# Optimization experiments

Measured on AMD Instinct MI355X. Metric: run time of the kernel, lower is better.

## Reference

```python
import jax, jax.numpy as jnp
import numpy as np

B, S, D = 1, 4096, 512
INNER = 512
K, PAD = 3, 1
MAX_OUT = 4 * S  # static padded output length (torch uses data-dependent max)
EPS = 1e-5
TINY_SLOWDOWN = 0.5


def _conv1d(x, w, b):
    # x: [B, C_in, S], w: [C_out, C_in, K] -> [B, C_out, S]
    y = jax.lax.conv_general_dilated(x, w, window_strides=(1,), padding=[(PAD, PAD)],
                                     dimension_numbers=('NCH', 'OIH', 'NCH'))
    return y + b[None, :, None]


def _layernorm(x, g, b):
    m = jnp.mean(x, axis=-1, keepdims=True)
    v = jnp.var(x, axis=-1, keepdims=True)
    return (x - m) * jax.lax.rsqrt(v + EPS) * g + b


def _duration_predictor(enc, c1w, c1b, g1, b1, c2w, c2b, g2, b2, lw, lb):
    # enc: [B, S, D]; dropout is identity (eval mode)
    x = _conv1d(enc.transpose(0, 2, 1), c1w, c1b).transpose(0, 2, 1)   # [B,S,INNER]
    x = jax.nn.relu(_layernorm(x, g1, b1))
    x = _conv1d(x.transpose(0, 2, 1), c2w, c2b).transpose(0, 2, 1)     # [B,S,INNER]
    x = jax.nn.relu(_layernorm(x, g2, b2))
    out = jax.nn.relu(jnp.einsum('bsd,od->bso', x, lw) + lb)           # [B,S,1]
    return out[..., 0]                                                  # [B,S] (B==1 => matches squeeze/unsqueeze(0))


def setup_inputs() -> dict:
    key = jax.random.key(0)
    ks = jax.random.split(key, 4)
    return {
        'enc_output': jax.random.normal(ks[0], (B, S, D), dtype=jnp.float32),
        'conv1_w': jax.random.normal(ks[1], (INNER, D, K), dtype=jnp.float32) * 0.02,
        'conv1_b': jnp.zeros((INNER,), jnp.float32),
        'ln1_g': jnp.ones((INNER,), jnp.float32),
        'ln1_b': jnp.zeros((INNER,), jnp.float32),
        'conv2_w': jax.random.normal(ks[2], (INNER, INNER, K), dtype=jnp.float32) * 0.02,
        'conv2_b': jnp.zeros((INNER,), jnp.float32),
        'ln2_g': jnp.ones((INNER,), jnp.float32),
        'ln2_b': jnp.zeros((INNER,), jnp.float32),
        'lin_w': jax.random.normal(ks[3], (1, INNER), jnp.float32) * 0.1,
        'lin_b': jnp.zeros((1,), jnp.float32),
    }


def reference(enc_output, conv1_w, conv1_b, ln1_g, ln1_b, conv2_w, conv2_b,
              ln2_g, ln2_b, lin_w, lin_b):
    pred = _duration_predictor(enc_output, conv1_w, conv1_b, ln1_g, ln1_b,
                               conv2_w, conv2_b, ln2_g, ln2_b, lin_w, lin_b)
    dur = jnp.floor(pred + TINY_SLOWDOWN).astype(jnp.int32)            # [B,S], nonneg so floor == int()
    cum = jnp.cumsum(dur, axis=-1)                                     # [B,S]
    t = jnp.arange(MAX_OUT, dtype=jnp.int32)                           # [T]
    # frame t belongs to phoneme i where cum[i-1] <= t < cum[i]
    idx = jax.vmap(lambda c: jnp.searchsorted(c, t, side='right'))(cum)  # [B,T]
    valid = t[None, :] < cum[:, -1:]                                   # [B,T]
    idx = jnp.clip(idx, 0, S - 1)
    gathered = jnp.take_along_axis(enc_output, idx[:, :, None], axis=1)  # [B,T,D]
    mod_enc_output = jnp.where(valid[:, :, None], gathered, jnp.zeros((), enc_output.dtype))
    output_pos = jnp.arange(1, MAX_OUT + 1, dtype=jnp.int64 if jax.config.jax_enable_x64 else jnp.int32)[None, :]
    return mod_enc_output, output_pos
```

## Files before the change

kernel.cpp:

```cpp
#include <hip/hip_runtime.h>

#define S      4096
#define D      512
#define KWIN   3
#define SP     (S + 2)
#define MAXOUT 16384
#define EPSLN  1e-5f
#define NIT    16
#define NKT    48
#define NPAIR  24

typedef __attribute__((ext_vector_type(8))) short short8;
typedef __attribute__((ext_vector_type(4))) float floatx4;

__device__ inline ushort f2bf(float x) {
  union { float f; unsigned u; } v; v.f = x;
  unsigned r = v.u + 0x7fffu + ((v.u >> 16) & 1u);
  return (ushort)(r >> 16);
}
__device__ inline float bf2f(ushort h) {
  union { float f; unsigned u; } v; v.u = ((unsigned)h) << 16;
  return v.f;
}

#define PBX 1025
#define PBW 384

__global__ __launch_bounds__(256) void pack_all_kernel(
    const float* __restrict__ x, const float* __restrict__ w1,
    const float* __restrict__ w2, ushort* __restrict__ Xph,
    ushort* __restrict__ Xpl, ushort* __restrict__ B1h, ushort* __restrict__ B1l,
    ushort* __restrict__ B2h, ushort* __restrict__ B2l,
    ushort* __restrict__ T1h, ushort* __restrict__ T1l) {
  const int b = blockIdx.x;
  if (b < PBX) {
    const int v = b * 256 + threadIdx.x;
    if (v >= SP * 64) return;
    const int g   = v >> 6;
    const int oct = v & 63;
    const int i0  = oct * 8;
    float vv[8];
    if (g == 0 || g == SP - 1) {
#pragma unroll
      for (int j = 0; j < 8; ++j) vv[j] = 0.f;
    } else {
      const float4 a = *(const float4*)(x + (size_t)(g - 1) * D + i0);
      const float4 c = *(const float4*)(x + (size_t)(g - 1) * D + i0 + 4);
      vv[0] = a.x; vv[1] = a.y; vv[2] = a.z; vv[3] = a.w;
      vv[4] = c.x; vv[5] = c.y; vv[6] = c.z; vv[7] = c.w;
    }
    short8 h8, l8;
#pragma unroll
    for (int j = 0; j < 8; ++j) {
      const ushort hi = f2bf(vv[j]);
      h8[j] = (short)hi;
      l8[j] = (short)f2bf(vv[j] - bf2f(hi));
    }
    const size_t dst = ((size_t)(oct >> 2) * SP + g) * 32 + (size_t)(oct & 3) * 8;
    *(short8*)(Xph + dst) = h8;
    *(short8*)(Xpl + dst) = l8;
  } else if (b < PBX + 2 * PBW) {
    const int wsel = (b - PBX) >= PBW;
    const int u = ((b - PBX) - (wsel ? PBW : 0)) * 256 + threadIdx.x;
    const float* __restrict__ w = wsel ? w2 : w1;
    ushort* __restrict__ bh = wsel ? B2h : B1h;
    ushort* __restrict__ bl = wsel ? B2l : B1l;
    const int kk0 = (u & 3) * 8;
    const int o   = (u >> 2) & 511;
    const int it  = (u >> 11) & 15;
    const int k   = u >> 15;
    const float* __restrict__ src =
        w + (size_t)o * (D * KWIN) + (size_t)(it * 32 + kk0) * KWIN + k;
    short8 h8, l8;
#pragma unroll
    for (int j = 0; j < 8; ++j) {
      const float vv = src[j * KWIN];
      const ushort hi = f2bf(vv);
      h8[j] = (short)hi;
      l8[j] = (short)f2bf(vv - bf2f(hi));
    }
    const size_t idx = (size_t)kk0 + ((size_t)o << 5) + ((size_t)it << 14) +
                       ((size_t)k << 18);
    *(short8*)(bh + idx) = h8;
    *(short8*)(bl + idx) = l8;
  } else {
    const int z = threadIdx.x;
    if (z < 128) {
      const int c    = z >> 3;
      const int rr   = (z >> 2) & 1;
      const int colo = (z & 3) * 8;
      const size_t off = ((size_t)c * SP + (rr ? (SP - 1) : 0)) * 32 + colo;
      short8 zero = {};
      *(short8*)(T1h + off) = zero;
      *(short8*)(T1l + off) = zero;
    }
  }
}

#define TM 128
#define TN 64
#define AH_OFF 0
#define AL_OFF 8192
#define BH_OFF 16384
#define BL_OFF 20480
#define DBUFSZ 24576

__device__ inline void gload16(const void* g, void* l) {
  __builtin_amdgcn_global_load_lds((const __attribute__((address_space(1))) void*)g,
                                   (__attribute__((address_space(3))) void*)l,
                                   16, 0, 0);
}

__global__ __launch_bounds__(512) void gemm_mfma_kernel(
    const ushort* __restrict__ Ah, const ushort* __restrict__ Al,
    const ushort* __restrict__ Bh, const ushort* __restrict__ Bl,
    float* __restrict__ C) {
  __shared__ __align__(16) ushort smem[2 * DBUFSZ];

  const int tid  = threadIdx.x;
  const int wave = tid >> 6;
  const int lane = tid & 63;
  const int row0 = blockIdx.x * TM;
  const int col0 = blockIdx.y * TN;
  const int wm0  = (wave >> 1) * 32;
  const int wn0  = (wave & 1) * 32;
  const int fr   = lane & 15;
  const int quad = lane >> 4;

  floatx4 acc[2][2] = {};

  auto stage = [&](int p, int db) {
    ushort* base = smem + db * DBUFSZ;
    if (wave < 4) {
      const int sub = wave & 1;
      const int kt  = 2 * p + sub;
      const int tap   = kt >> 4;
      const int itile = kt & 15;
      const ushort* gb = (wave < 2 ? Ah : Al) +
                         ((size_t)itile * SP + row0 + tap) * 32;
      ushort* lb = base + (wave < 2 ? AH_OFF : AL_OFF) + sub * 4096;
#pragma unroll
      for (int seg = 0; seg < 8; ++seg)
        gload16(gb + seg * 512 + lane * 8, lb + seg * 512);
    } else if (wave < 6) {
      const ushort* src = (wave == 4 ? Bh : Bl);
      ushort* lb0 = base + (wave == 4 ? BH_OFF : BL_OFF);
#pragma unroll
      for (int sub = 0; sub < 2; ++sub) {
        const int kt = 2 * p + sub;
        const ushort* gb = src + ((size_t)kt * D + col0) * 32;
#pragma unroll
        for (int seg = 0; seg < 4; ++seg)
          gload16(gb + seg * 512 + lane * 8, lb0 + sub * 2048 + seg * 512);
      }
    }
  };

  stage(0, 0);

  for (int p = 0; p < NPAIR; ++p) {
    const int db = p & 1;
    __syncthreads();
    if (p + 1 < NPAIR) stage(p + 1, db ^ 1);

#pragma unroll
    for (int sub = 0; sub < 2; ++sub) {
      short8 ah[2], al2[2], bh[2], bl2[2];
#pragma unroll
      for (int mf = 0; mf < 2; ++mf) {
        const int off = sub * 4096 + (wm0 + mf * 16 + fr) * 32 + quad * 8;
        ah[mf]  = *(const short8*)&smem[db * DBUFSZ + AH_OFF + off];
        al2[mf] = *(const short8*)&smem[db * DBUFSZ + AL_OFF + off];
      }
#pragma unroll
      for (int nf = 0; nf < 2; ++nf) {
        const int offb = sub * 2048 + (wn0 + nf * 16 + fr) * 32 + quad * 8;
        bh[nf]  = *(const short8*)&smem[db * DBUFSZ + BH_OFF + offb];
        bl2[nf] = *(const short8*)&smem[db * DBUFSZ + BL_OFF + offb];
      }
#pragma unroll
      for (int mf = 0; mf < 2; ++mf)
#pragma unroll
        for (int nf = 0; nf < 2; ++nf) {
          acc[mf][nf] = __builtin_amdgcn_mfma_f32_16x16x32_bf16(ah[mf],  bh[nf],  acc[mf][nf], 0, 0, 0);
          acc[mf][nf] = __builtin_amdgcn_mfma_f32_16x16x32_bf16(ah[mf],  bl2[nf], acc[mf][nf], 0, 0, 0);
          acc[mf][nf] = __builtin_amdgcn_mfma_f32_16x16x32_bf16(al2[mf], bh[nf],  acc[mf][nf], 0, 0, 0);
        }
    }
  }

#pragma unroll
  for (int mf = 0; mf < 2; ++mf)
#pragma unroll
    for (int nf = 0; nf < 2; ++nf) {
      const int col = col0 + wn0 + nf * 16 + fr;
#pragma unroll
      for (int r = 0; r < 4; ++r) {
        const int row = row0 + wm0 + mf * 16 + quad * 4 + r;
        C[(size_t)row * D + col] = acc[mf][nf][r];
      }
    }
}

__global__ __launch_bounds__(256) void ln_relu_pack_kernel(
    const float* __restrict__ X, const float* __restrict__ cb,
    const float* __restrict__ gam, const float* __restrict__ bet,
    ushort* __restrict__ th, ushort* __restrict__ tl) {
  const int wave = threadIdx.x >> 6;
  const int lane = threadIdx.x & 63;
  const int s = blockIdx.x * 4 + wave;
  const float4* xp = (const float4*)(X + (size_t)s * D);
  float4 a = xp[2 * lane];
  float4 b = xp[2 * lane + 1];
  const float4 ca  = ((const float4*)cb)[2 * lane];
  const float4 cb2 = ((const float4*)cb)[2 * lane + 1];
  float v[8] = {a.x + ca.x,  a.y + ca.y,  a.z + ca.z,  a.w + ca.w,
                b.x + cb2.x, b.y + cb2.y, b.z + cb2.z, b.w + cb2.w};
  float sum = 0.f;
#pragma unroll
  for (int i = 0; i < 8; ++i) sum += v[i];
#pragma unroll
  for (int off = 32; off > 0; off >>= 1) sum += __shfl_xor(sum, off);
  const float m = sum * (1.0f / D);
  float sq = 0.f;
#pragma unroll
  for (int i = 0; i < 8; ++i) { v[i] -= m; sq += v[i] * v[i]; }
#pragma unroll
  for (int off = 32; off > 0; off >>= 1) sq += __shfl_xor(sq, off);
  const float rs = rsqrtf(sq * (1.0f / D) + EPSLN);
  const float4 ga = ((const float4*)gam)[2 * lane];
  const float4 gb = ((const float4*)gam)[2 * lane + 1];
  const float4 ba = ((const float4*)bet)[2 * lane];
  const float4 bb = ((const float4*)bet)[2 * lane + 1];
  const float gg[8] = {ga.x, ga.y, ga.z, ga.w, gb.x, gb.y, gb.z, gb.w};
  const float bt[8] = {ba.x, ba.y, ba.z, ba.w, bb.x, bb.y, bb.z, bb.w};
  short8 h8, l8;
#pragma unroll
  for (int i = 0; i < 8; ++i) {
    float y = fmaxf(v[i] * rs * gg[i] + bt[i], 0.0f);
    ushort hi = f2bf(y);
    h8[i] = (short)hi;
    l8[i] = (short)f2bf(y - bf2f(hi));
  }
  const size_t base = ((size_t)(lane >> 2) * SP + (s + 1)) * 32 + (size_t)(lane & 3) * 8;
  *(short8*)(th + base) = h8;
  *(short8*)(tl + base) = l8;
}

__global__ __launch_bounds__(256) void ln2_pred_kernel(
    const float* __restrict__ X, const float* __restrict__ cb,
    const float* __restrict__ gam, const float* __restrict__ bet,
    const float* __restrict__ lw, const float* __restrict__ lb,
    int* __restrict__ dur) {
  const int wave = threadIdx.x >> 6;
  const int lane = threadIdx.x & 63;
  const int s = blockIdx.x * 4 + wave;
  const float4* xp = (const float4*)(X + (size_t)s * D);
  float4 a = xp[2 * lane];
  float4 b = xp[2 * lane + 1];
  const float4 ca  = ((const float4*)cb)[2 * lane];
  const float4 cb2 = ((const float4*)cb)[2 * lane + 1];
  float v[8] = {a.x + ca.x,  a.y + ca.y,  a.z + ca.z,  a.w + ca.w,
                b.x + cb2.x, b.y + cb2.y, b.z + cb2.z, b.w + cb2.w};
  float sum = 0.f;
#pragma unroll
  for (int i = 0; i < 8; ++i) sum += v[i];
#pragma unroll
  for (int off = 32; off > 0; off >>= 1) sum += __shfl_xor(sum, off);
  const float m = sum * (1.0f / D);
  float sq = 0.f;
#pragma unroll
  for (int i = 0; i < 8; ++i) { v[i] -= m; sq += v[i] * v[i]; }
#pragma unroll
  for (int off = 32; off > 0; off >>= 1) sq += __shfl_xor(sq, off);
  const float rs = rsqrtf(sq * (1.0f / D) + EPSLN);
  const float4 ga = ((const float4*)gam)[2 * lane];
  const float4 gb = ((const float4*)gam)[2 * lane + 1];
  const float4 ba = ((const float4*)bet)[2 * lane];
  const float4 bb = ((const float4*)bet)[2 * lane + 1];
  const float gg[8] = {ga.x, ga.y, ga.z, ga.w, gb.x, gb.y, gb.z, gb.w};
  const float bt[8] = {ba.x, ba.y, ba.z, ba.w, bb.x, bb.y, bb.z, bb.w};
  const float4 w0 = ((const float4*)lw)[2 * lane];
  const float4 w1 = ((const float4*)lw)[2 * lane + 1];
  const float ww[8] = {w0.x, w0.y, w0.z, w0.w, w1.x, w1.y, w1.z, w1.w};
  float d = 0.f;
#pragma unroll
  for (int i = 0; i < 8; ++i) {
    float y = fmaxf(v[i] * rs * gg[i] + bt[i], 0.0f);
    d += y * ww[i];
  }
#pragma unroll
  for (int off = 32; off > 0; off >>= 1) d += __shfl_xor(d, off);
  if (lane == 0) {
    const float p = fmaxf(d + lb[0], 0.0f);
    dur[s] = (int)floorf(p + 0.5f);
  }
}

__global__ __launch_bounds__(64) void scan_kernel(const int* __restrict__ dur,
                                                  int* __restrict__ cum) {
  const int lane = threadIdx.x;
  const int4* src = (const int4*)dur + (size_t)lane * 16;
  int4 v[16];
  int run = 0;
#pragma unroll
  for (int i = 0; i < 16; ++i) {
    int4 d = src[i];
    d.x += run; d.y += d.x; d.z += d.y; d.w += d.z;
    run = d.w;
    v[i] = d;
  }
  int sc = run;
#pragma unroll
  for (int off = 1; off < 64; off <<= 1) {
    const int n = __shfl_up(sc, off);
    if (lane >= off) sc += n;
  }
  const int base = sc - run;
  int4* dst = (int4*)cum + (size_t)lane * 16;
#pragma unroll
  for (int i = 0; i < 16; ++i) {
    int4 d = v[i];
    d.x += base; d.y += base; d.z += base; d.w += base;
    dst[i] = d;
  }
}

__global__ __launch_bounds__(256) void gather_kernel(
    const float* __restrict__ enc, const int* __restrict__ cum,
    float* __restrict__ out0, float* __restrict__ out1) {
  const int half = threadIdx.x >> 7;
  const int d4   = (threadIdx.x & 127) << 2;
  const int t    = blockIdx.x * 2 + half;
  const int total = cum[S - 1];

  int lo = 0, hi = S;
  while (lo < hi) {
    const int mid = (lo + hi) >> 1;
    if (cum[mid] <= t) lo = mid + 1; else hi = mid;
  }
  const int idx = (lo < S) ? lo : (S - 1);

  float4 v = make_float4(0.f, 0.f, 0.f, 0.f);
  if (t < total) v = *(const float4*)(enc + (size_t)idx * D + d4);
  *(float4*)(out0 + (size_t)t * D + d4) = v;

  if ((threadIdx.x & 127) == 0) out1[t] = (float)(t + 1);
}

extern "C" void kernel_launch(void* const* d_in, const int* in_sizes, int n_in,
                              void* d_out, int out_size, void* d_ws, size_t ws_size,
                              hipStream_t stream) {
  const float* enc = (const float*)d_in[0];
  const float* w1  = (const float*)d_in[1];
  const float* cb1 = (const float*)d_in[2];
  const float* g1  = (const float*)d_in[3];
  const float* be1 = (const float*)d_in[4];
  const float* w2  = (const float*)d_in[5];
  const float* cb2 = (const float*)d_in[6];
  const float* g2  = (const float*)d_in[7];
  const float* be2 = (const float*)d_in[8];
  const float* lw  = (const float*)d_in[9];
  const float* lb  = (const float*)d_in[10];

  float* out0 = (float*)d_out;
  float* out1 = out0 + (size_t)MAXOUT * D;

  const size_t NP = (size_t)NIT * SP * 32;
  const size_t NB = (size_t)NKT * D * 32;
  ushort* Xph = (ushort*)d_ws;
  ushort* Xpl = Xph + NP;
  ushort* T1h = Xpl + NP;
  ushort* T1l = T1h + NP;
  ushort* B1h = T1l + NP;
  ushort* B1l = B1h + NB;
  ushort* B2h = B1l + NB;
  ushort* B2l = B2h + NB;
  float*  t0  = (float*)(B2l + NB);
  int*   dur  = (int*)(t0 + (size_t)S * D);
  int*   cum  = dur + S;

  pack_all_kernel<<<PBX + 2 * PBW + 1, 256, 0, stream>>>(
      enc, w1, w2, Xph, Xpl, B1h, B1l, B2h, B2l, T1h, T1l);
  gemm_mfma_kernel<<<dim3(S / TM, D / TN), 512, 0, stream>>>(Xph, Xpl, B1h, B1l, t0);
  ln_relu_pack_kernel<<<S / 4, 256, 0, stream>>>(t0, cb1, g1, be1, T1h, T1l);
  gemm_mfma_kernel<<<dim3(S / TM, D / TN), 512, 0, stream>>>(T1h, T1l, B2h, B2l, t0);
  ln2_pred_kernel<<<S / 4, 256, 0, stream>>>(t0, cb2, g2, be2, lw, lb, dur);
  scan_kernel<<<1, 64, 0, stream>>>(dur, cum);
  gather_kernel<<<MAXOUT / 2, 256, 0, stream>>>(enc, cum, out0, out1);
}
```

Before: 169.4 us.

## Split GEMM waves along K with LDS reduction and fuse scan via last-block ticket

In the GEMM, waves now each cover the full 64-column N tile over one of the two K sub-tiles. Each pass loads a wider set of B fragments, and the two K halves are summed through shared memory before the store. The goal is to cut redundant LDS fragment reads per MFMA, at the cost of an extra reduction step and twice as many accumulator registers. Separately, the scan kernel is folded into the ln2/prediction kernel using an atomic ticket so the last block does the prefix sum. This removes one kernel launch but adds an atomic and threadfences.

New measurement: 222.4 us. 1.31x slower.

```diff
diff --git a/kernel.cpp b/kernel.cpp
--- a/kernel.cpp
+++ b/kernel.cpp
@@ -31,7 +31,8 @@
     const float* __restrict__ w2, ushort* __restrict__ Xph,
     ushort* __restrict__ Xpl, ushort* __restrict__ B1h, ushort* __restrict__ B1l,
     ushort* __restrict__ B2h, ushort* __restrict__ B2l,
-    ushort* __restrict__ T1h, ushort* __restrict__ T1l) {
+    ushort* __restrict__ T1h, ushort* __restrict__ T1l,
+    int* __restrict__ cnt) {
   const int b = blockIdx.x;
   if (b < PBX) {
     const int v = b * 256 + threadIdx.x;
@@ -93,6 +94,8 @@
       short8 zero = {};
       *(short8*)(T1h + off) = zero;
       *(short8*)(T1l + off) = zero;
+    } else if (z == 128) {
+      cnt[0] = 0;
     }
   }
 }
@@ -120,14 +123,15 @@
   const int tid  = threadIdx.x;
   const int wave = tid >> 6;
   const int lane = tid & 63;
+  const int ms   = wave >> 1;
+  const int kh   = wave & 1;
   const int row0 = blockIdx.x * TM;
   const int col0 = blockIdx.y * TN;
-  const int wm0  = (wave >> 1) * 32;
-  const int wn0  = (wave & 1) * 32;
+  const int wm0  = ms * 32;
   const int fr   = lane & 15;
   const int quad = lane >> 4;
 
-  floatx4 acc[2][2] = {};
+  floatx4 acc[2][4] = {};
 
   auto stage = [&](int p, int db) {
     ushort* base = smem + db * DBUFSZ;
@@ -158,48 +162,64 @@
 
   stage(0, 0);
 
+  const int soa = kh * 4096;
+  const int sob = kh * 2048;
+
   for (int p = 0; p < NPAIR; ++p) {
     const int db = p & 1;
     __syncthreads();
     if (p + 1 < NPAIR) stage(p + 1, db ^ 1);
 
-#pragma unroll
-    for (int sub = 0; sub < 2; ++sub) {
-      short8 ah[2], al2[2], bh[2], bl2[2];
-#pragma unroll
-      for (int mf = 0; mf < 2; ++mf) {
-        const int off = sub * 4096 + (wm0 + mf * 16 + fr) * 32 + quad * 8;
-        ah[mf]  = *(const short8*)&smem[db * DBUFSZ + AH_OFF + off];
-        al2[mf] = *(const short8*)&smem[db * DBUFSZ + AL_OFF + off];
+    const int dbo = db * DBUFSZ;
+    short8 ah[2], al2[2], bh[4], bl2[4];
+#pragma unroll
+    for (int mf = 0; mf < 2; ++mf) {
+      const int off = soa + (wm0 + mf * 16 + fr) * 32 + quad * 8;
+      ah[mf]  = *(const short8*)&smem[dbo + AH_OFF + off];
+      al2[mf] = *(const short8*)&smem[dbo + AL_OFF + off];
+    }
+#pragma unroll
+    for (int nf = 0; nf < 4; ++nf) {
+      const int offb = sob + (nf * 16 + fr) * 32 + quad * 8;
+      bh[nf]  = *(const short8*)&smem[dbo + BH_OFF + offb];
+      bl2[nf] = *(const short8*)&smem[dbo + BL_OFF + offb];
+    }
+#pragma unroll
+    for (int mf = 0; mf < 2; ++mf)
+#pragma unroll
+      for (int nf = 0; nf < 4; ++nf) {
+        acc[mf][nf] = __builtin_amdgcn_mfma_f32_16x16x32_bf16(ah[mf],  bh[nf],  acc[mf][nf], 0, 0, 0);
+        acc[mf][nf] = __builtin_amdgcn_mfma_f32_16x16x32_bf16(ah[mf],  bl2[nf], acc[mf][nf], 0, 0, 0);
+        acc[mf][nf] = __builtin_amdgcn_mfma_f32_16x16x32_bf16(al2[mf], bh[nf],  acc[mf][nf], 0, 0, 0);
       }
-#pragma unroll
-      for (int nf = 0; nf < 2; ++nf) {
-        const int offb = sub * 2048 + (wn0 + nf * 16 + fr) * 32 + quad * 8;
-        bh[nf]  = *(const short8*)&smem[db * DBUFSZ + BH_OFF + offb];
-        bl2[nf] = *(const short8*)&smem[db * DBUFSZ + BL_OFF + offb];
+  }
+
+  __syncthreads();
+  float* red = (float*)smem;
+  if (kh == 1) {
+#pragma unroll
+    for (int mf = 0; mf < 2; ++mf)
+#pragma unroll
+      for (int nf = 0; nf < 4; ++nf)
+        *(floatx4*)&red[((((ms * 2 + mf) * 4 + nf) * 64) + lane) * 4] = acc[mf][nf];
+  }
+  __syncthreads();
+  if (kh == 0) {
+#pragma unroll
+    for (int mf = 0; mf < 2; ++mf)
+#pragma unroll
+      for (int nf = 0; nf < 4; ++nf) {
+        const floatx4 o =
+            *(const floatx4*)&red[((((ms * 2 + mf) * 4 + nf) * 64) + lane) * 4];
+        acc[mf][nf] += o;
+        const int col = col0 + nf * 16 + fr;
+#pragma unroll
+        for (int r = 0; r < 4; ++r) {
+          const int row = row0 + wm0 + mf * 16 + quad * 4 + r;
+          C[(size_t)row * D + col] = acc[mf][nf][r];
+        }
       }
-#pragma unroll
-      for (int mf = 0; mf < 2; ++mf)
-#pragma unroll
-        for (int nf = 0; nf < 2; ++nf) {
-          acc[mf][nf] = __builtin_amdgcn_mfma_f32_16x16x32_bf16(ah[mf],  bh[nf],  acc[mf][nf], 0, 0, 0);
-          acc[mf][nf] = __builtin_amdgcn_mfma_f32_16x16x32_bf16(ah[mf],  bl2[nf], acc[mf][nf], 0, 0, 0);
-          acc[mf][nf] = __builtin_amdgcn_mfma_f32_16x16x32_bf16(al2[mf], bh[nf],  acc[mf][nf], 0, 0, 0);
-        }
-    }
-  }
-
-#pragma unroll
-  for (int mf = 0; mf < 2; ++mf)
-#pragma unroll
-    for (int nf = 0; nf < 2; ++nf) {
-      const int col = col0 + wn0 + nf * 16 + fr;
-#pragma unroll
-      for (int r = 0; r < 4; ++r) {
-        const int row = row0 + wm0 + mf * 16 + quad * 4 + r;
-        C[(size_t)row * D + col] = acc[mf][nf][r];
-      }
-    }
+  }
 }
 
 __global__ __launch_bounds__(256) void ln_relu_pack_kernel(
@@ -247,11 +267,11 @@
   *(short8*)(tl + base) = l8;
 }
 
-__global__ __launch_bounds__(256) void ln2_pred_kernel(
+__global__ __launch_bounds__(256) void ln2_pred_scan_kernel(
     const float* __restrict__ X, const float* __restrict__ cb,
     const float* __restrict__ gam, const float* __restrict__ bet,
     const float* __restrict__ lw, const float* __restrict__ lb,
-    int* __restrict__ dur) {
+    int* __restrict__ dur, int* __restrict__ cum, int* __restrict__ cnt) {
   const int wave = threadIdx.x >> 6;
   const int lane = threadIdx.x & 63;
   const int s = blockIdx.x * 4 + wave;
@@ -295,34 +315,39 @@
     const float p = fmaxf(d + lb[0], 0.0f);
     dur[s] = (int)floorf(p + 0.5f);
   }
-}
-
-__global__ __launch_bounds__(64) void scan_kernel(const int* __restrict__ dur,
-                                                  int* __restrict__ cum) {
-  const int lane = threadIdx.x;
-  const int4* src = (const int4*)dur + (size_t)lane * 16;
-  int4 v[16];
+
+  __syncthreads();
+  __threadfence();
+  __shared__ int ticket;
+  if (threadIdx.x == 0) ticket = atomicAdd(cnt, 1);
+  __syncthreads();
+  if (ticket != (S / 4) - 1) return;
+  __threadfence();
+  if (threadIdx.x >= 64) return;
+  const int l = threadIdx.x;
+  const int4* src = (const int4*)dur + (size_t)l * 16;
+  int4 vv[16];
   int run = 0;
 #pragma unroll
   for (int i = 0; i < 16; ++i) {
-    int4 d = src[i];
-    d.x += run; d.y += d.x; d.z += d.y; d.w += d.z;
-    run = d.w;
-    v[i] = d;
+    int4 dd = src[i];
+    dd.x += run; dd.y += dd.x; dd.z += dd.y; dd.w += dd.z;
+    run = dd.w;
+    vv[i] = dd;
   }
   int sc = run;
 #pragma unroll
   for (int off = 1; off < 64; off <<= 1) {
     const int n = __shfl_up(sc, off);
-    if (lane >= off) sc += n;
+    if (l >= off) sc += n;
   }
   const int base = sc - run;
-  int4* dst = (int4*)cum + (size_t)lane * 16;
+  int4* dst = (int4*)cum + (size_t)l * 16;
 #pragma unroll
   for (int i = 0; i < 16; ++i) {
-    int4 d = v[i];
-    d.x += base; d.y += base; d.z += base; d.w += base;
-    dst[i] = d;
+    int4 dd = vv[i];
+    dd.x += base; dd.y += base; dd.z += base; dd.w += base;
+    dst[i] = dd;
   }
 }
 
@@ -379,13 +404,13 @@
   float*  t0  = (float*)(B2l + NB);
   int*   dur  = (int*)(t0 + (size_t)S * D);
   int*   cum  = dur + S;
+  int*   cnt  = cum + S;
 
   pack_all_kernel<<<PBX + 2 * PBW + 1, 256, 0, stream>>>(
-      enc, w1, w2, Xph, Xpl, B1h, B1l, B2h, B2l, T1h, T1l);
+      enc, w1, w2, Xph, Xpl, B1h, B1l, B2h, B2l, T1h, T1l, cnt);
   gemm_mfma_kernel<<<dim3(S / TM, D / TN), 512, 0, stream>>>(Xph, Xpl, B1h, B1l, t0);
   ln_relu_pack_kernel<<<S / 4, 256, 0, stream>>>(t0, cb1, g1, be1, T1h, T1l);
   gemm_mfma_kernel<<<dim3(S / TM, D / TN), 512, 0, stream>>>(T1h, T1l, B2h, B2l, t0);
-  ln2_pred_kernel<<<S / 4, 256, 0, stream>>>(t0, cb2, g2, be2, lw, lb, dur);
-  scan_kernel<<<1, 64, 0, stream>>>(dur, cum);
+  ln2_pred_scan_kernel<<<S / 4, 256, 0, stream>>>(t0, cb2, g2, be2, lw, lb, dur, cum, cnt);
   gather_kernel<<<MAXOUT / 2, 256, 0, stream>>>(enc, cum, out0, out1);
 }
```

## Split K across wave pairs in GEMM with LDS reduction of partial sums

Applied to the files above, without the earlier changes.

Changes the GEMM wave decomposition so each wave pair splits the two K sub-tiles instead of the N dimension. Each wave now computes a 32x64 output tile over half the K slices, which cuts LDS fragment reads per MFMA. The two partial accumulators are then summed through shared memory before the store. This adds an end-of-kernel reduction with two barriers, doubles the accumulator registers, and leaves half the waves idle during the store.

Measured after the change: 163.4 us (median of 2 runs). 1.04x faster.

```diff
diff --git a/kernel.cpp b/kernel.cpp
--- a/kernel.cpp
+++ b/kernel.cpp
@@ -120,14 +120,15 @@
   const int tid  = threadIdx.x;
   const int wave = tid >> 6;
   const int lane = tid & 63;
+  const int ms   = wave >> 1;
+  const int kh   = wave & 1;
   const int row0 = blockIdx.x * TM;
   const int col0 = blockIdx.y * TN;
-  const int wm0  = (wave >> 1) * 32;
-  const int wn0  = (wave & 1) * 32;
+  const int wm0  = ms * 32;
   const int fr   = lane & 15;
   const int quad = lane >> 4;
 
-  floatx4 acc[2][2] = {};
+  floatx4 acc[2][4] = {};
 
   auto stage = [&](int p, int db) {
     ushort* base = smem + db * DBUFSZ;
@@ -158,48 +159,64 @@
 
   stage(0, 0);
 
+  const int soa = kh * 4096;
+  const int sob = kh * 2048;
+
   for (int p = 0; p < NPAIR; ++p) {
     const int db = p & 1;
     __syncthreads();
     if (p + 1 < NPAIR) stage(p + 1, db ^ 1);
 
-#pragma unroll
-    for (int sub = 0; sub < 2; ++sub) {
-      short8 ah[2], al2[2], bh[2], bl2[2];
-#pragma unroll
-      for (int mf = 0; mf < 2; ++mf) {
-        const int off = sub * 4096 + (wm0 + mf * 16 + fr) * 32 + quad * 8;
-        ah[mf]  = *(const short8*)&smem[db * DBUFSZ + AH_OFF + off];
-        al2[mf] = *(const short8*)&smem[db * DBUFSZ + AL_OFF + off];
+    const int dbo = db * DBUFSZ;
+    short8 ah[2], al2[2], bh[4], bl2[4];
+#pragma unroll
+    for (int mf = 0; mf < 2; ++mf) {
+      const int off = soa + (wm0 + mf * 16 + fr) * 32 + quad * 8;
+      ah[mf]  = *(const short8*)&smem[dbo + AH_OFF + off];
+      al2[mf] = *(const short8*)&smem[dbo + AL_OFF + off];
+    }
+#pragma unroll
+    for (int nf = 0; nf < 4; ++nf) {
+      const int offb = sob + (nf * 16 + fr) * 32 + quad * 8;
+      bh[nf]  = *(const short8*)&smem[dbo + BH_OFF + offb];
+      bl2[nf] = *(const short8*)&smem[dbo + BL_OFF + offb];
+    }
+#pragma unroll
+    for (int mf = 0; mf < 2; ++mf)
+#pragma unroll
+      for (int nf = 0; nf < 4; ++nf) {
+        acc[mf][nf] = __builtin_amdgcn_mfma_f32_16x16x32_bf16(ah[mf],  bh[nf],  acc[mf][nf], 0, 0, 0);
+        acc[mf][nf] = __builtin_amdgcn_mfma_f32_16x16x32_bf16(ah[mf],  bl2[nf], acc[mf][nf], 0, 0, 0);
+        acc[mf][nf] = __builtin_amdgcn_mfma_f32_16x16x32_bf16(al2[mf], bh[nf],  acc[mf][nf], 0, 0, 0);
       }
-#pragma unroll
-      for (int nf = 0; nf < 2; ++nf) {
-        const int offb = sub * 2048 + (wn0 + nf * 16 + fr) * 32 + quad * 8;
-        bh[nf]  = *(const short8*)&smem[db * DBUFSZ + BH_OFF + offb];
-        bl2[nf] = *(const short8*)&smem[db * DBUFSZ + BL_OFF + offb];
+  }
+
+  __syncthreads();
+  float* red = (float*)smem;
+  if (kh == 1) {
+#pragma unroll
+    for (int mf = 0; mf < 2; ++mf)
+#pragma unroll
+      for (int nf = 0; nf < 4; ++nf)
+        *(floatx4*)&red[((((ms * 2 + mf) * 4 + nf) * 64) + lane) * 4] = acc[mf][nf];
+  }
+  __syncthreads();
+  if (kh == 0) {
+#pragma unroll
+    for (int mf = 0; mf < 2; ++mf)
+#pragma unroll
+      for (int nf = 0; nf < 4; ++nf) {
+        const floatx4 o =
+            *(const floatx4*)&red[((((ms * 2 + mf) * 4 + nf) * 64) + lane) * 4];
+        acc[mf][nf] += o;
+        const int col = col0 + nf * 16 + fr;
+#pragma unroll
+        for (int r = 0; r < 4; ++r) {
+          const int row = row0 + wm0 + mf * 16 + quad * 4 + r;
+          C[(size_t)row * D + col] = acc[mf][nf][r];
+        }
       }
-#pragma unroll
-      for (int mf = 0; mf < 2; ++mf)
-#pragma unroll
-        for (int nf = 0; nf < 2; ++nf) {
-          acc[mf][nf] = __builtin_amdgcn_mfma_f32_16x16x32_bf16(ah[mf],  bh[nf],  acc[mf][nf], 0, 0, 0);
-          acc[mf][nf] = __builtin_amdgcn_mfma_f32_16x16x32_bf16(ah[mf],  bl2[nf], acc[mf][nf], 0, 0, 0);
-          acc[mf][nf] = __builtin_amdgcn_mfma_f32_16x16x32_bf16(al2[mf], bh[nf],  acc[mf][nf], 0, 0, 0);
-        }
-    }
-  }
-
-#pragma unroll
-  for (int mf = 0; mf < 2; ++mf)
-#pragma unroll
-    for (int nf = 0; nf < 2; ++nf) {
-      const int col = col0 + wn0 + nf * 16 + fr;
-#pragma unroll
-      for (int r = 0; r < 4; ++r) {
-        const int row = row0 + wm0 + mf * 16 + quad * 4 + r;
-        C[(size_t)row * D + col] = acc[mf][nf][r];
-      }
-    }
+  }
 }
 
 __global__ __launch_bounds__(256) void ln_relu_pack_kernel(
```

## Switch GEMM to 32x32x16 MFMA with split-K across waves and LDS reduction

Applied to the files above, without the earlier changes.

The conv GEMM kernel now uses 32x32x16 bf16 MFMA tiles. The 8 waves are split into 2 row groups by 4 K-slices, so each wave covers the full 128x64 tile slice for its K portion. Partial accumulators from three of the four K-groups are written to shared memory and summed by the kq==0 waves before the store. The aim is to cut LDS fragment loads per MFMA and use the larger, more efficient MFMA shape. In exchange it adds a reduction epilogue with extra syncs, LDS traffic and more accumulator registers.

Result: no change. 172.2 us (+1.6%).

```diff
diff --git a/kernel.cpp b/kernel.cpp
--- a/kernel.cpp
+++ b/kernel.cpp
@@ -12,6 +12,7 @@
 
 typedef __attribute__((ext_vector_type(8))) short short8;
 typedef __attribute__((ext_vector_type(4))) float floatx4;
+typedef __attribute__((ext_vector_type(16))) float f32x16;
 
 __device__ inline ushort f2bf(float x) {
   union { float f; unsigned u; } v; v.f = x;
@@ -120,25 +121,26 @@
   const int tid  = threadIdx.x;
   const int wave = tid >> 6;
   const int lane = tid & 63;
+  const int ms2  = wave & 1;
+  const int kq   = wave >> 1;
   const int row0 = blockIdx.x * TM;
   const int col0 = blockIdx.y * TN;
-  const int wm0  = (wave >> 1) * 32;
-  const int wn0  = (wave & 1) * 32;
-  const int fr   = lane & 15;
-  const int quad = lane >> 4;
-
-  floatx4 acc[2][2] = {};
+  const int l31  = lane & 31;
+  const int koff = (kq & 1) * 16 + (lane >> 5) * 8;
+  const int sub  = kq >> 1;
+
+  f32x16 acc[2][2] = {};
 
   auto stage = [&](int p, int db) {
     ushort* base = smem + db * DBUFSZ;
     if (wave < 4) {
-      const int sub = wave & 1;
-      const int kt  = 2 * p + sub;
+      const int ssub = wave & 1;
+      const int kt  = 2 * p + ssub;
       const int tap   = kt >> 4;
       const int itile = kt & 15;
       const ushort* gb = (wave < 2 ? Ah : Al) +
                          ((size_t)itile * SP + row0 + tap) * 32;
-      ushort* lb = base + (wave < 2 ? AH_OFF : AL_OFF) + sub * 4096;
+      ushort* lb = base + (wave < 2 ? AH_OFF : AL_OFF) + ssub * 4096;
 #pragma unroll
       for (int seg = 0; seg < 8; ++seg)
         gload16(gb + seg * 512 + lane * 8, lb + seg * 512);
@@ -146,12 +148,12 @@
       const ushort* src = (wave == 4 ? Bh : Bl);
       ushort* lb0 = base + (wave == 4 ? BH_OFF : BL_OFF);
 #pragma unroll
-      for (int sub = 0; sub < 2; ++sub) {
-        const int kt = 2 * p + sub;
+      for (int ssub = 0; ssub < 2; ++ssub) {
+        const int kt = 2 * p + ssub;
         const ushort* gb = src + ((size_t)kt * D + col0) * 32;
 #pragma unroll
         for (int seg = 0; seg < 4; ++seg)
-          gload16(gb + seg * 512 + lane * 8, lb0 + sub * 2048 + seg * 512);
+          gload16(gb + seg * 512 + lane * 8, lb0 + ssub * 2048 + seg * 512);
       }
     }
   };
@@ -163,43 +165,80 @@
     __syncthreads();
     if (p + 1 < NPAIR) stage(p + 1, db ^ 1);
 
-#pragma unroll
-    for (int sub = 0; sub < 2; ++sub) {
-      short8 ah[2], al2[2], bh[2], bl2[2];
-#pragma unroll
-      for (int mf = 0; mf < 2; ++mf) {
-        const int off = sub * 4096 + (wm0 + mf * 16 + fr) * 32 + quad * 8;
-        ah[mf]  = *(const short8*)&smem[db * DBUFSZ + AH_OFF + off];
-        al2[mf] = *(const short8*)&smem[db * DBUFSZ + AL_OFF + off];
+    const int dbo = db * DBUFSZ;
+    short8 a_h[2], a_l[2], b_h[2], b_l[2];
+#pragma unroll
+    for (int rt = 0; rt < 2; ++rt) {
+      const int off = sub * 4096 + (ms2 * 64 + rt * 32 + l31) * 32 + koff;
+      a_h[rt] = *(const short8*)&smem[dbo + AH_OFF + off];
+      a_l[rt] = *(const short8*)&smem[dbo + AL_OFF + off];
+    }
+#pragma unroll
+    for (int ct = 0; ct < 2; ++ct) {
+      const int offb = sub * 2048 + (ct * 32 + l31) * 32 + koff;
+      b_h[ct] = *(const short8*)&smem[dbo + BH_OFF + offb];
+      b_l[ct] = *(const short8*)&smem[dbo + BL_OFF + offb];
+    }
+#pragma unroll
+    for (int rt = 0; rt < 2; ++rt)
+#pragma unroll
+      for (int ct = 0; ct < 2; ++ct) {
+        acc[rt][ct] = __builtin_amdgcn_mfma_f32_32x32x16_bf16(a_h[rt], b_h[ct], acc[rt][ct], 0, 0, 0);
+        acc[rt][ct] = __builtin_amdgcn_mfma_f32_32x32x16_bf16(a_h[rt], b_l[ct], acc[rt][ct], 0, 0, 0);
+        acc[rt][ct] = __builtin_amdgcn_mfma_f32_32x32x16_bf16(a_l[rt], b_h[ct], acc[rt][ct], 0, 0, 0);
       }
-#pragma unroll
-      for (int nf = 0; nf < 2; ++nf) {
-        const int offb = sub * 2048 + (wn0 + nf * 16 + fr) * 32 + quad * 8;
-        bh[nf]  = *(const short8*)&smem[db * DBUFSZ + BH_OFF + offb];
-        bl2[nf] = *(const short8*)&smem[db * DBUFSZ + BL_OFF + offb];
+  }
+
+  __syncthreads();
+  float* red = (float*)smem;
+  if (kq != 0) {
+    const int idx = ((kq - 1) * 2 + ms2) * 4096;
+#pragma unroll
+    for (int rt = 0; rt < 2; ++rt)
+#pragma unroll
+      for (int ct = 0; ct < 2; ++ct)
+#pragma unroll
+        for (int q = 0; q < 4; ++q) {
+          floatx4 v;
+          v[0] = acc[rt][ct][q * 4 + 0];
+          v[1] = acc[rt][ct][q * 4 + 1];
+          v[2] = acc[rt][ct][q * 4 + 2];
+          v[3] = acc[rt][ct][q * 4 + 3];
+          *(floatx4*)&red[idx + (rt * 2 + ct) * 1024 + q * 256 + lane * 4] = v;
+        }
+  }
+  __syncthreads();
+  if (kq == 0) {
+#pragma unroll
+    for (int k2 = 1; k2 < 4; ++k2) {
+      const int idx = ((k2 - 1) * 2 + ms2) * 4096;
+#pragma unroll
+      for (int rt = 0; rt < 2; ++rt)
+#pragma unroll
+        for (int ct = 0; ct < 2; ++ct)
+#pragma unroll
+          for (int q = 0; q < 4; ++q) {
+            const floatx4 v =
+                *(const floatx4*)&red[idx + (rt * 2 + ct) * 1024 + q * 256 + lane * 4];
+            acc[rt][ct][q * 4 + 0] += v[0];
+            acc[rt][ct][q * 4 + 1] += v[1];
+            acc[rt][ct][q * 4 + 2] += v[2];
+            acc[rt][ct][q * 4 + 3] += v[3];
+          }
+    }
+    const int rbase = row0 + ms2 * 64 + 4 * (lane >> 5);
+#pragma unroll
+    for (int rt = 0; rt < 2; ++rt)
+#pragma unroll
+      for (int ct = 0; ct < 2; ++ct) {
+        const int col = col0 + ct * 32 + l31;
+#pragma unroll
+        for (int reg = 0; reg < 16; ++reg) {
+          const int row = rbase + rt * 32 + (reg & 3) + 8 * (reg >> 2);
+          C[(size_t)row * D + col] = acc[rt][ct][reg];
+        }
       }
-#pragma unroll
-      for (int mf = 0; mf < 2; ++mf)
-#pragma unroll
-        for (int nf = 0; nf < 2; ++nf) {
-          acc[mf][nf] = __builtin_amdgcn_mfma_f32_16x16x32_bf16(ah[mf],  bh[nf],  acc[mf][nf], 0, 0, 0);
-          acc[mf][nf] = __builtin_amdgcn_mfma_f32_16x16x32_bf16(ah[mf],  bl2[nf], acc[mf][nf], 0, 0, 0);
-          acc[mf][nf] = __builtin_amdgcn_mfma_f32_16x16x32_bf16(al2[mf], bh[nf],  acc[mf][nf], 0, 0, 0);
-        }
-    }
-  }
-
-#pragma unroll
-  for (int mf = 0; mf < 2; ++mf)
-#pragma unroll
-    for (int nf = 0; nf < 2; ++nf) {
-      const int col = col0 + wn0 + nf * 16 + fr;
-#pragma unroll
-      for (int r = 0; r < 4; ++r) {
-        const int row = row0 + wm0 + mf * 16 + quad * 4 + r;
-        C[(size_t)row * D + col] = acc[mf][nf][r];
-      }
-    }
+  }
 }
 
 __global__ __launch_bounds__(256) void ln_relu_pack_kernel(
```
